# Kernel tuning notes

Hardware: AMD Instinct MI355X
Metric: run time of the kernel (lower is better)

Reference implementation:

```python
import jax, jax.numpy as jnp
import numpy as np

B, D, M, R, C = 4096, 16, 4, 2048, 10
EPS = 1e-9


def setup_inputs() -> dict:
    key = jax.random.key(0)
    k1, k2, k3, k4, k5 = jax.random.split(key, 5)
    x = jax.random.normal(k1, (B, D), dtype=jnp.float32)
    centers = jax.random.normal(k2, (D, M), dtype=jnp.float32)
    widths = jax.random.uniform(k3, (D, M), dtype=jnp.float32, minval=0.5, maxval=1.5)
    consequents = jax.random.uniform(k4, (R, D + 1, C), dtype=jnp.float32)
    rules = jax.random.randint(k5, (R, D), 0, M, dtype=jnp.int32)
    return {"x": x, "centers": centers, "widths": widths,
            "consequents": consequents, "rules": rules}


def reference(x, centers, widths, consequents, rules):
    batch = x.shape[0]
    # Gaussian membership values: (B, D, M)
    mfs = jnp.exp(-((x[:, :, None] - centers[None]) ** 2) / (2.0 * widths[None] ** 2))
    # Gather per-rule memberships: rule_mfs[b, d, r] = mfs[b, d, rules[r, d]] -> (B, D, R)
    idx = jnp.broadcast_to(rules.T[None].astype(jnp.int32), (batch, rules.shape[1], rules.shape[0]))
    rule_mfs = jnp.take_along_axis(mfs, idx, axis=2)
    # Firing strengths: product over input dims -> (B, R)
    fs = jnp.prod(rule_mfs, axis=1)
    norm_fs = fs / (jnp.sum(fs, axis=1, keepdims=True) + EPS)
    # Extended input with bias column -> (B, D+1)
    x_ext = jnp.concatenate([x, jnp.ones((batch, 1), dtype=x.dtype)], axis=1)
    # Faithful to torch.einsum('bi,rjc->brc', ...): i and j are both summed out
    rule_vals = jnp.einsum('bi,rjc->brc', x_ext, consequents)  # (B, R, C)
    out = jnp.einsum('br,brc->bc', norm_fs, rule_vals)  # (B, C)
    return out, norm_fs, x_ext
```

## Files before the change

### kernel.cpp

```cpp
#include <hip/hip_runtime.h>

#define BB 4096
#define DD 16
#define MM 4
#define RR 2048
#define CC 10
#define TB 2
#define RPT (RR / 256)

typedef __attribute__((ext_vector_type(4))) float f32x4;
typedef __attribute__((ext_vector_type(2))) float f32x2;

__global__ __launch_bounds__(256) void prep_kernel(
    const float* __restrict__ cons, const int* __restrict__ rules,
    float* __restrict__ wsum4a, float* __restrict__ wsum4b,
    float* __restrict__ wsum2, unsigned int* __restrict__ codes)
{
    int gid = blockIdx.x * 256 + threadIdx.x;
    if (gid < RR * CC) {
        int r = gid / CC, c = gid - r * CC;
        const float* cr = cons + (size_t)r * (DD + 1) * CC + c;
        float s = 0.0f;
#pragma unroll
        for (int j = 0; j < DD + 1; ++j) s += cr[j * CC];
        if (c < 4)      wsum4a[r * 4 + c] = s;
        else if (c < 8) wsum4b[r * 4 + (c - 4)] = s;
        else            wsum2[r * 2 + (c - 8)] = s;
    }
    if (gid < RR) {
        const int* rrp = rules + gid * DD;
        unsigned int code = 0;
#pragma unroll
        for (int g = 0; g < 4; ++g) {
            unsigned int byt = 0;
#pragma unroll
            for (int k = 0; k < 4; ++k)
                byt |= (((unsigned int)rrp[g * 4 + k]) & 3u) << (2 * k);
            code |= byt << (8 * g);
        }
        codes[gid] = code;
    }
}

__global__ __launch_bounds__(256, 8) void anfis_main(
    const float* __restrict__ x, const float* __restrict__ centers,
    const float* __restrict__ widths, const f32x4* __restrict__ wsum4a,
    const f32x4* __restrict__ wsum4b, const f32x2* __restrict__ wsum2,
    const unsigned int* __restrict__ codes,
    float* __restrict__ out, float* __restrict__ norm_fs, float* __restrict__ x_ext)
{
    __shared__ __align__(16) char pool[4 * 256 * sizeof(f32x2)];
    f32x2 (*Q2)[256] = (f32x2 (*)[256])pool;
    float (*RED)[68] = (float (*)[68])pool;

    __shared__ float MF[TB][64];
    __shared__ f32x2 PAIR2[8][16];
    __shared__ float xs[TB][DD];
    __shared__ float sx[TB];
    __shared__ float wpart[4][TB];
    __shared__ float invl[TB];
    __shared__ float oscale[TB];
    __shared__ float part2[TB * CC][4];

    const int tid = threadIdx.x;
    const int b0 = blockIdx.x * TB;
    const int lane = tid & 63;
    const int wv = tid >> 6;

    if (tid < TB * (DD + 1)) {
        int row = tid / (DD + 1), col = tid % (DD + 1);
        float v = (col < DD) ? x[(b0 + row) * DD + col] : 1.0f;
        if (col < DD) xs[row][col] = v;
        x_ext[(b0 + row) * (DD + 1) + col] = v;
    }
    __syncthreads();
    if (tid < TB) {
        float s = 1.0f;
#pragma unroll
        for (int d = 0; d < DD; ++d) s += xs[tid][d];
        sx[tid] = s;
    }

    if (tid < TB * 64) {
        int row = tid >> 6, dm = tid & 63, d = dm >> 2, m = dm & 3;
        float c = centers[d * MM + m];
        float w = widths[d * MM + m];
        float z = xs[row][d] - c;
        MF[row][dm] = expf(-(z * z) / (2.0f * w * w));
    }
    __syncthreads();

    if (tid < 8 * 16) {
        int p = tid >> 4, e = tid & 15;
        int i0 = e & 3, i1 = e >> 2;
        f32x2 v;
        v.x = MF[0][(2 * p) * 4 + i0] * MF[0][(2 * p + 1) * 4 + i1];
        v.y = MF[1][(2 * p) * 4 + i0] * MF[1][(2 * p + 1) * 4 + i1];
        PAIR2[p][e] = v;
    }
    __syncthreads();

#pragma unroll
    for (int i = tid; i < 4 * 256; i += 256) {
        int g = i >> 8, e = i & 255;
        Q2[g][e] = PAIR2[2 * g][e & 15] * PAIR2[2 * g + 1][e >> 4];
    }
    __syncthreads();

    float ssum0 = 0.0f, ssum1 = 0.0f;
#pragma unroll 1
    for (int j = 0; j < RPT; ++j) {
        unsigned int code = codes[tid + 256 * j];
        f32x2 q0 = Q2[0][code & 255u];
        f32x2 q1 = Q2[1][(code >> 8) & 255u];
        f32x2 q2 = Q2[2][(code >> 16) & 255u];
        f32x2 q3 = Q2[3][code >> 24];
        f32x2 p = (q0 * q1) * (q2 * q3);
        ssum0 += p.x;
        ssum1 += p.y;
    }

    {
        float s0 = ssum0, s1 = ssum1;
#pragma unroll
        for (int off = 32; off > 0; off >>= 1) {
            s0 += __shfl_xor(s0, off, 64);
            s1 += __shfl_xor(s1, off, 64);
        }
        if (lane == 0) { wpart[wv][0] = s0; wpart[wv][1] = s1; }
    }
    __syncthreads();
    if (tid < TB) {
        float t = wpart[0][tid] + wpart[1][tid] + wpart[2][tid] + wpart[3][tid];
        float inv = 1.0f / (t + 1e-9f);
        invl[tid] = inv;
        oscale[tid] = sx[tid] * inv;
    }
    __syncthreads();

    const float inv0 = invl[0], inv1 = invl[1];

    float acc[TB][CC];
#pragma unroll
    for (int row = 0; row < TB; ++row)
#pragma unroll
        for (int c = 0; c < CC; ++c) acc[row][c] = 0.0f;

#pragma unroll 1
    for (int j = 0; j < RPT; ++j) {
        int r = tid + 256 * j;
        unsigned int code = codes[r];
        f32x2 q0 = Q2[0][code & 255u];
        f32x2 q1 = Q2[1][(code >> 8) & 255u];
        f32x2 q2 = Q2[2][(code >> 16) & 255u];
        f32x2 q3 = Q2[3][code >> 24];
        f32x2 p = (q0 * q1) * (q2 * q3);

        norm_fs[(size_t)(b0 + 0) * RR + r] = p.x * inv0;
        norm_fs[(size_t)(b0 + 1) * RR + r] = p.y * inv1;

        const f32x4 wa = wsum4a[r];
        const f32x4 wb = wsum4b[r];
        const f32x2 wcp = wsum2[r];
        const float wc[CC] = {wa.x, wa.y, wa.z, wa.w, wb.x,
                              wb.y, wb.z, wb.w, wcp.x, wcp.y};
#pragma unroll
        for (int c = 0; c < CC; ++c) {
            acc[0][c] = fmaf(p.x, wc[c], acc[0][c]);
            acc[1][c] = fmaf(p.y, wc[c], acc[1][c]);
        }
    }
    __syncthreads();

#pragma unroll
    for (int row = 0; row < TB; ++row) {
#pragma unroll
        for (int c = 0; c < CC; ++c) {
            float s = acc[row][c];
            s += __shfl_xor(s, 1, 64);
            s += __shfl_xor(s, 2, 64);
            if ((lane & 3) == 0) RED[row * CC + c][wv * 16 + (lane >> 2)] = s;
        }
    }
    __syncthreads();
    if (tid < 80) {
        int v = tid % 20, ch = tid / 20;
        float s = 0.0f;
        int base = ch * 16;
#pragma unroll
        for (int i = 0; i < 16; ++i) s += RED[v][base + i];
        part2[v][ch] = s;
    }
    __syncthreads();
    if (tid < TB * CC) {
        float val = part2[tid][0] + part2[tid][1] + part2[tid][2] + part2[tid][3];
        int row = tid / CC, c = tid % CC;
        out[(b0 + row) * CC + c] = oscale[row] * val;
    }
}

extern "C" void kernel_launch(void* const* d_in, const int* in_sizes, int n_in,
                              void* d_out, int out_size, void* d_ws, size_t ws_size,
                              hipStream_t stream) {
    const float* x       = (const float*)d_in[0];
    const float* centers = (const float*)d_in[1];
    const float* widths  = (const float*)d_in[2];
    const float* cons    = (const float*)d_in[3];
    const int*   rules   = (const int*)d_in[4];

    float* out_p     = (float*)d_out;
    float* norm_fs_p = out_p + (size_t)BB * CC;
    float* x_ext_p   = norm_fs_p + (size_t)BB * RR;

    float* wsum4a = (float*)d_ws;
    float* wsum4b = wsum4a + (size_t)RR * 4;
    float* wsum2  = wsum4b + (size_t)RR * 4;
    unsigned int* codes = (unsigned int*)(wsum2 + (size_t)RR * 2);

    prep_kernel<<<(RR * CC + 255) / 256, 256, 0, stream>>>(cons, rules, wsum4a,
                                                           wsum4b, wsum2, codes);
    anfis_main<<<BB / TB, 256, 0, stream>>>(x, centers, widths,
                                            (const f32x4*)wsum4a,
                                            (const f32x4*)wsum4b,
                                            (const f32x2*)wsum2, codes,
                                            out_p, norm_fs_p, x_ext_p);
}
```

Baseline: 89.55 us.

## Fuse firing-strength passes, batch four rows per block, stash strengths in LDS as bf16

Each block now handles four batch rows instead of two, carrying four lanes of products through the shared-memory quad tables. The firing-strength sum and the consequent accumulation happen in one rule loop. Strengths are kept in LDS as packed bf16, so the second loop only scales them and writes norm_fs. This removes the recomputation of the gathered products and the second read of the consequent sums, and halves the block count. In exchange it uses more registers and LDS per block, and rounding norm_fs through bf16 loses precision against the reference.

New measurement: 86.74 us. -3.1%, faster.

```diff
diff --git a/kernel.cpp b/kernel.cpp
--- a/kernel.cpp
+++ b/kernel.cpp
@@ -5,11 +5,22 @@
 #define MM 4
 #define RR 2048
 #define CC 10
-#define TB 2
+#define TB 4
 #define RPT (RR / 256)
 
 typedef __attribute__((ext_vector_type(4))) float f32x4;
 typedef __attribute__((ext_vector_type(2))) float f32x2;
+typedef __attribute__((ext_vector_type(4))) unsigned short u16x4;
+
+__device__ __forceinline__ unsigned short f2bf(float x) {
+    union { float f; unsigned u; } v; v.f = x;
+    unsigned b = v.u + 0x7FFFu + ((v.u >> 16) & 1u);
+    return (unsigned short)(b >> 16);
+}
+__device__ __forceinline__ float bf2f(unsigned short h) {
+    union { unsigned u; float f; } v; v.u = ((unsigned)h) << 16;
+    return v.f;
+}
 
 __global__ __launch_bounds__(256) void prep_kernel(
     const float* __restrict__ cons, const int* __restrict__ rules,
@@ -42,19 +53,20 @@
     }
 }
 
-__global__ __launch_bounds__(256, 8) void anfis_main(
+__global__ __launch_bounds__(256, 4) void anfis_main(
     const float* __restrict__ x, const float* __restrict__ centers,
     const float* __restrict__ widths, const f32x4* __restrict__ wsum4a,
     const f32x4* __restrict__ wsum4b, const f32x2* __restrict__ wsum2,
     const unsigned int* __restrict__ codes,
     float* __restrict__ out, float* __restrict__ norm_fs, float* __restrict__ x_ext)
 {
-    __shared__ __align__(16) char pool[4 * 256 * sizeof(f32x2)];
-    f32x2 (*Q2)[256] = (f32x2 (*)[256])pool;
-    float (*RED)[68] = (float (*)[68])pool;
-
+    __shared__ __align__(16) char pool[4 * 256 * sizeof(f32x4)];
+    f32x4 (*QUAD4)[256] = (f32x4 (*)[256])pool;
+    float (*RED)[68]    = (float (*)[68])pool;
+
+    __shared__ u16x4 FS[RR];
     __shared__ float MF[TB][64];
-    __shared__ f32x2 PAIR2[8][16];
+    __shared__ f32x4 PAIR4[8][16];
     __shared__ float xs[TB][DD];
     __shared__ float sx[TB];
     __shared__ float wpart[4][TB];
@@ -81,7 +93,7 @@
         sx[tid] = s;
     }
 
-    if (tid < TB * 64) {
+    {
         int row = tid >> 6, dm = tid & 63, d = dm >> 2, m = dm & 3;
         float c = centers[d * MM + m];
         float w = widths[d * MM + m];
@@ -93,41 +105,63 @@
     if (tid < 8 * 16) {
         int p = tid >> 4, e = tid & 15;
         int i0 = e & 3, i1 = e >> 2;
-        f32x2 v;
-        v.x = MF[0][(2 * p) * 4 + i0] * MF[0][(2 * p + 1) * 4 + i1];
-        v.y = MF[1][(2 * p) * 4 + i0] * MF[1][(2 * p + 1) * 4 + i1];
-        PAIR2[p][e] = v;
+        f32x4 v;
+#pragma unroll
+        for (int row = 0; row < TB; ++row)
+            v[row] = MF[row][(2 * p) * 4 + i0] * MF[row][(2 * p + 1) * 4 + i1];
+        PAIR4[p][e] = v;
     }
     __syncthreads();
 
 #pragma unroll
     for (int i = tid; i < 4 * 256; i += 256) {
         int g = i >> 8, e = i & 255;
-        Q2[g][e] = PAIR2[2 * g][e & 15] * PAIR2[2 * g + 1][e >> 4];
-    }
-    __syncthreads();
-
-    float ssum0 = 0.0f, ssum1 = 0.0f;
+        QUAD4[g][e] = PAIR4[2 * g][e & 15] * PAIR4[2 * g + 1][e >> 4];
+    }
+    __syncthreads();
+
+    float acc[TB][CC];
+#pragma unroll
+    for (int row = 0; row < TB; ++row)
+#pragma unroll
+        for (int c = 0; c < CC; ++c) acc[row][c] = 0.0f;
+
+    f32x4 svec = {0.0f, 0.0f, 0.0f, 0.0f};
+
 #pragma unroll 1
     for (int j = 0; j < RPT; ++j) {
-        unsigned int code = codes[tid + 256 * j];
-        f32x2 q0 = Q2[0][code & 255u];
-        f32x2 q1 = Q2[1][(code >> 8) & 255u];
-        f32x2 q2 = Q2[2][(code >> 16) & 255u];
-        f32x2 q3 = Q2[3][code >> 24];
-        f32x2 p = (q0 * q1) * (q2 * q3);
-        ssum0 += p.x;
-        ssum1 += p.y;
-    }
-
-    {
-        float s0 = ssum0, s1 = ssum1;
-#pragma unroll
-        for (int off = 32; off > 0; off >>= 1) {
-            s0 += __shfl_xor(s0, off, 64);
-            s1 += __shfl_xor(s1, off, 64);
-        }
-        if (lane == 0) { wpart[wv][0] = s0; wpart[wv][1] = s1; }
+        int r = tid + 256 * j;
+        unsigned int code = codes[r];
+        f32x4 q0 = QUAD4[0][code & 255u];
+        f32x4 q1 = QUAD4[1][(code >> 8) & 255u];
+        f32x4 q2 = QUAD4[2][(code >> 16) & 255u];
+        f32x4 q3 = QUAD4[3][code >> 24];
+        f32x4 p = (q0 * q1) * (q2 * q3);
+        svec += p;
+
+        u16x4 fh;
+        fh.x = f2bf(p[0]); fh.y = f2bf(p[1]);
+        fh.z = f2bf(p[2]); fh.w = f2bf(p[3]);
+        FS[r] = fh;
+
+        const f32x4 wa = wsum4a[r];
+        const f32x4 wb = wsum4b[r];
+        const f32x2 wcp = wsum2[r];
+        const float wc[CC] = {wa.x, wa.y, wa.z, wa.w, wb.x,
+                              wb.y, wb.z, wb.w, wcp.x, wcp.y};
+#pragma unroll
+        for (int row = 0; row < TB; ++row)
+#pragma unroll
+            for (int c = 0; c < CC; ++c)
+                acc[row][c] = fmaf(p[row], wc[c], acc[row][c]);
+    }
+
+#pragma unroll
+    for (int row = 0; row < TB; ++row) {
+        float s = svec[row];
+#pragma unroll
+        for (int off = 32; off > 0; off >>= 1) s += __shfl_xor(s, off, 64);
+        if (lane == 0) wpart[wv][row] = s;
     }
     __syncthreads();
     if (tid < TB) {
@@ -138,39 +172,17 @@
     }
     __syncthreads();
 
-    const float inv0 = invl[0], inv1 = invl[1];
-
-    float acc[TB][CC];
-#pragma unroll
-    for (int row = 0; row < TB; ++row)
-#pragma unroll
-        for (int c = 0; c < CC; ++c) acc[row][c] = 0.0f;
+    const float inv0 = invl[0], inv1 = invl[1], inv2 = invl[2], inv3 = invl[3];
 
 #pragma unroll 1
     for (int j = 0; j < RPT; ++j) {
         int r = tid + 256 * j;
-        unsigned int code = codes[r];
-        f32x2 q0 = Q2[0][code & 255u];
-        f32x2 q1 = Q2[1][(code >> 8) & 255u];
-        f32x2 q2 = Q2[2][(code >> 16) & 255u];
-        f32x2 q3 = Q2[3][code >> 24];
-        f32x2 p = (q0 * q1) * (q2 * q3);
-
-        norm_fs[(size_t)(b0 + 0) * RR + r] = p.x * inv0;
-        norm_fs[(size_t)(b0 + 1) * RR + r] = p.y * inv1;
-
-        const f32x4 wa = wsum4a[r];
-        const f32x4 wb = wsum4b[r];
-        const f32x2 wcp = wsum2[r];
-        const float wc[CC] = {wa.x, wa.y, wa.z, wa.w, wb.x,
-                              wb.y, wb.z, wb.w, wcp.x, wcp.y};
-#pragma unroll
-        for (int c = 0; c < CC; ++c) {
-            acc[0][c] = fmaf(p.x, wc[c], acc[0][c]);
-            acc[1][c] = fmaf(p.y, wc[c], acc[1][c]);
-        }
-    }
-    __syncthreads();
+        u16x4 fh = FS[r];
+        norm_fs[(size_t)(b0 + 0) * RR + r] = bf2f(fh.x) * inv0;
+        norm_fs[(size_t)(b0 + 1) * RR + r] = bf2f(fh.y) * inv1;
+        norm_fs[(size_t)(b0 + 2) * RR + r] = bf2f(fh.z) * inv2;
+        norm_fs[(size_t)(b0 + 3) * RR + r] = bf2f(fh.w) * inv3;
+    }
 
 #pragma unroll
     for (int row = 0; row < TB; ++row) {
@@ -183,8 +195,8 @@
         }
     }
     __syncthreads();
-    if (tid < 80) {
-        int v = tid % 20, ch = tid / 20;
+    if (tid < 160) {
+        int v = tid % 40, ch = tid / 40;
         float s = 0.0f;
         int base = ch * 16;
 #pragma unroll
```
